# Kernel tuning notes

Hardware: AMD Instinct MI355X
Metric: run time of the kernel (lower is better)

Reference implementation:

```python
import jax, jax.numpy as jnp
import numpy as np

WD, WH, WW = 1, 8, 8           # window size
NH = 2                          # num heads
EPS = 1e-5                      # torch LayerNorm default


def _layernorm(x, g, b):
    mu = jnp.mean(x, axis=-1, keepdims=True)
    var = jnp.mean((x - mu) ** 2, axis=-1, keepdims=True)
    return (x - mu) * jax.lax.rsqrt(var + EPS) * g + b


def setup_inputs() -> dict:
    key = jax.random.key(0)
    ks = jax.random.split(key, 12)
    C, H = 192, 768  # dim, mlp hidden
    w = lambda k, shape: (jax.random.normal(k, shape, jnp.float32) * 0.02)
    return {
        "x": jax.random.normal(ks[0], (2, 8, 96, 96, C), jnp.float32),
        "norm3_g": jnp.ones((C,), jnp.float32),
        "norm3_b": jnp.zeros((C,), jnp.float32),
        "in_proj_w": w(ks[1], (3 * C, C)),
        "in_proj_b": jnp.zeros((3 * C,), jnp.float32),
        "out_proj_w": w(ks[2], (C, C)),
        "out_proj_b": jnp.zeros((C,), jnp.float32),
        "norm4_g": jnp.ones((C,), jnp.float32),
        "norm4_b": jnp.zeros((C,), jnp.float32),
        "fc1_w": w(ks[3], (H, C)),
        "fc1_b": jnp.zeros((H,), jnp.float32),
        "fc2_w": w(ks[4], (C, H)),
        "fc2_b": jnp.zeros((C,), jnp.float32),
    }


def _part3(x, norm3_g, norm3_b, in_proj_w, in_proj_b, out_proj_w, out_proj_b):
    B, D, H, W, C = x.shape
    Dn, Hn, Wn = D // WD, H // WH, W // WW
    P = Hn * Wn          # spatial windows
    Wt = WD * WH * WW    # tokens per window (64)
    L = Dn * Wt          # attention sequence length

    xn = _layernorm(x, norm3_g, norm3_b)
    # window partition: (B, Dn, Hn, Wn, wd, wh, ww, C)
    xw = xn.reshape(B, Dn, WD, Hn, WH, Wn, WW, C).transpose(0, 1, 3, 5, 2, 4, 6, 7)
    # tgt: (B, Dn, P, Wt, C) -> h: (B*P, Dn*Wt, C)
    tgt = xw.reshape(B, Dn, P, Wt, C)
    h = tgt.transpose(0, 2, 1, 3, 4).reshape(B * P, L, C)

    # qkv projection (torch Linear convention: x @ W.T + b)
    qkv = h @ in_proj_w.T + in_proj_b          # (Bp, L, 3C)
    q, k, v = jnp.split(qkv, 3, axis=-1)
    hd = C // NH
    q = q.reshape(B * P, L, NH, hd)
    k = k.reshape(B * P, L, NH, hd)
    v = v.reshape(B * P, L, NH, hd)

    # block-causal mask over temporal index (each block is Wt x Wt)
    neg_inf = jnp.finfo(jnp.float32).min
    tmask = jnp.triu(jnp.full((Dn, Dn), neg_inf, jnp.float32), k=1)
    mask = jnp.repeat(jnp.repeat(tmask, Wt, axis=0), Wt, axis=1)  # (L, L)

    scale = 1.0 / np.sqrt(hd)
    scores = jnp.einsum("blhd,bmhd->bhlm", q * scale, k) + mask
    attn = jax.nn.softmax(scores, axis=-1)
    out = jnp.einsum("bhlm,bmhd->blhd", attn, v).reshape(B * P, L, C)
    out = out @ out_proj_w.T + out_proj_b

    # reverse: (B, P, Dn, Wt, C) -> windows -> (B, D, H, W, C)
    out = out.reshape(B, P, Dn, Wt, C).transpose(0, 2, 1, 3, 4)
    out = out.reshape(B, Dn, Hn, Wn, WD, WH, WW, C)
    out = out.transpose(0, 1, 4, 2, 5, 3, 6, 7).reshape(B, D, H, W, C)
    return out


def reference(x, norm3_g, norm3_b, in_proj_w, in_proj_b, out_proj_w, out_proj_b,
              norm4_g, norm4_b, fc1_w, fc1_b, fc2_w, fc2_b):
    x = x + _part3(x, norm3_g, norm3_b, in_proj_w, in_proj_b, out_proj_w, out_proj_b)
    xn = _layernorm(x, norm4_g, norm4_b)
    mlp = jax.nn.gelu(xn @ fc1_w.T + fc1_b, approximate=False) @ fc2_w.T + fc2_b
    return x + mlp
```

## Files before the change

kernel.cpp:

```cpp
#include <hip/hip_runtime.h>
#include <cstdint>
#include <cstddef>


typedef float   f32x4  __attribute__((ext_vector_type(4)));
typedef __bf16  bf16x8 __attribute__((ext_vector_type(8)));
typedef unsigned int   u32x4  __attribute__((ext_vector_type(4)));
typedef unsigned short u16x4  __attribute__((ext_vector_type(4)));

#define DEVI __device__ __forceinline__

DEVI float bf2f(unsigned short u) {
    union { unsigned int i; float f; } v; v.i = ((unsigned int)u) << 16; return v.f;
}
DEVI unsigned short f2bf(float f) {
    unsigned int u = __builtin_bit_cast(unsigned int, f);
    unsigned int r = u + 0x7fffu + ((u >> 16) & 1u);
    return (unsigned short)(r >> 16);
}
DEVI float gelu_sig(float v) {
    float e = __expf(-1.702f * v);
    return v * __builtin_amdgcn_rcpf(1.f + e);
}
DEVI unsigned int pk_fp8x4(float a, float b, float c, float d) {
    int v = __builtin_amdgcn_cvt_pk_fp8_f32(a, b, 0, false);
    v = __builtin_amdgcn_cvt_pk_fp8_f32(c, d, v, true);
    return (unsigned int)v;
}
DEVI f32x4 mfma_fp8(unsigned long long a, unsigned long long b, f32x4 c) {
    return __builtin_amdgcn_mfma_f32_16x16x32_fp8_fp8((long)a, (long)b, c, 0, 0, 0);
}

typedef __attribute__((address_space(3))) unsigned char       lds_u8;
typedef __attribute__((address_space(1))) const unsigned char g_u8;
DEVI void gl_lds16(const void* g, void* l) {
    __builtin_amdgcn_global_load_lds((g_u8*)g, (lds_u8*)l, 16, 0, 0);
}

__global__ __launch_bounds__(256) void k_wconv(const float* __restrict__ wqkv,
                                               const float* __restrict__ wout,
                                               const float* __restrict__ wfc1,
                                               const float* __restrict__ wfc2,
                                               const float* __restrict__ n3g,
                                               const float* __restrict__ n4g,
                                               unsigned short* __restrict__ oq,
                                               unsigned short* __restrict__ oo,
                                               unsigned short* __restrict__ o1,
                                               unsigned short* __restrict__ o2f8) {
    int i = blockIdx.x * 256 + threadIdx.x;
    if (i < 122880) {
        int r = i / 192, c = i - r * 192;
        oq[i] = (r < 576) ? f2bf(wqkv[i] * n3g[c]) : (unsigned short)0;
    } else if (i < 172032) {
        int j = i - 122880; int r = j / 192;
        oo[j] = (r < 192) ? f2bf(wout[j]) : (unsigned short)0;
    } else if (i < 319488) {
        int j = i - 172032; int c = j % 192;
        o1[j] = f2bf(wfc1[j] * n4g[c]);
    } else if (i < 417792) {
        int j = i - 319488;
        int r = j / 384;
        float a = 0.f, b = 0.f;
        if (r < 192) { a = wfc2[2 * j]; b = wfc2[2 * j + 1]; }
        int pk = __builtin_amdgcn_cvt_pk_fp8_f32(a, b, 0, false);
        o2f8[j] = (unsigned short)pk;
    }
}

__global__ __launch_bounds__(256) void k_bias(const float* __restrict__ wqkv,
                                              const float* __restrict__ bqkv,
                                              const float* __restrict__ n3b,
                                              const float* __restrict__ wfc1,
                                              const float* __restrict__ bfc1,
                                              const float* __restrict__ n4b,
                                              float* __restrict__ beffq,
                                              float* __restrict__ beff1) {
    int wid = blockIdx.x * 4 + (threadIdx.x >> 6);
    int lane = threadIdx.x & 63;
    const float* wrow; const float* bb; float base; float* dst;
    if (wid < 576) { wrow = wqkv + (size_t)wid * 192; bb = n3b; base = bqkv[wid]; dst = beffq + wid; }
    else { int h = wid - 576; wrow = wfc1 + (size_t)h * 192; bb = n4b; base = bfc1[h]; dst = beff1 + h; }
    float s = wrow[lane] * bb[lane] + wrow[lane + 64] * bb[lane + 64]
            + wrow[lane + 128] * bb[lane + 128];
#pragma unroll
    for (int off = 32; off; off >>= 1) s += __shfl_xor(s, off);
    if (lane == 0) *dst = base + s;
}

__global__ __launch_bounds__(256) void k_ln3(const float* __restrict__ x,
                                             unsigned short* __restrict__ h) {
    int w = threadIdx.x >> 6, lane = threadIdx.x & 63;
    int token = blockIdx.x * 4 + w;
    const float* xp = x + (size_t)token * 192;
    float v0 = xp[lane], v1 = xp[lane + 64], v2 = xp[lane + 128];
    float s = v0 + v1 + v2;
#pragma unroll
    for (int off = 32; off; off >>= 1) s += __shfl_xor(s, off);
    float mean = s * (1.f / 192.f);
    float d0 = v0 - mean, d1 = v1 - mean, d2 = v2 - mean;
    float q = d0 * d0 + d1 * d1 + d2 * d2;
#pragma unroll
    for (int off = 32; off; off >>= 1) q += __shfl_xor(q, off);
    float rs = rsqrtf(q * (1.f / 192.f) + 1e-5f);
    int b  = token / (8 * 96 * 96);
    int r0 = token - b * (8 * 96 * 96);
    int d  = r0 / (96 * 96);
    int r1 = r0 - d * (96 * 96);
    int hh = r1 / 96;
    int ww = r1 - hh * 96;
    int bp = b * 144 + (hh >> 3) * 12 + (ww >> 3);
    int l  = d * 64 + (hh & 7) * 8 + (ww & 7);
    unsigned short* hp = h + ((size_t)bp * 512 + l) * 192;
    hp[lane]       = f2bf(d0 * rs);
    hp[lane + 64]  = f2bf(d1 * rs);
    hp[lane + 128] = f2bf(d2 * rs);
}

__global__ __launch_bounds__(256) void k_ln4b(const unsigned short* __restrict__ yb,
                                              unsigned short* __restrict__ xn) {
    int sub = threadIdx.x >> 5, tl = threadIdx.x & 31;
    size_t row = (size_t)blockIdx.x * 8 + sub;
    const unsigned int* rp = reinterpret_cast<const unsigned int*>(yb + row * 192);
    float v[6];
#pragma unroll
    for (int j = 0; j < 3; j++) {
        unsigned int w = rp[tl + 32 * j];
        v[2 * j]     = bf2f((unsigned short)(w & 0xffffu));
        v[2 * j + 1] = bf2f((unsigned short)(w >> 16));
    }
    float s = v[0] + v[1] + v[2] + v[3] + v[4] + v[5];
#pragma unroll
    for (int off = 1; off < 32; off <<= 1) s += __shfl_xor(s, off);
    float mean = s * (1.f / 192.f);
    float q = 0.f;
#pragma unroll
    for (int j = 0; j < 6; j++) { v[j] -= mean; q += v[j] * v[j]; }
#pragma unroll
    for (int off = 1; off < 32; off <<= 1) q += __shfl_xor(q, off);
    float rs = rsqrtf(q * (1.f / 192.f) + 1e-5f);
    unsigned int* op = reinterpret_cast<unsigned int*>(xn + row * 192);
#pragma unroll
    for (int j = 0; j < 3; j++) {
        unsigned short lo = f2bf(v[2 * j]     * rs);
        unsigned short hi = f2bf(v[2 * j + 1] * rs);
        op[tl + 32 * j] = ((unsigned int)hi << 16) | lo;
    }
}

template <int EPI, int K, int NF>
__global__ __launch_bounds__(256) void k_gemm128(const unsigned short* __restrict__ A,
                                                 const unsigned short* __restrict__ Bw,
                                                 const float* __restrict__ bias,
                                                 unsigned short* __restrict__ outb,
                                                 unsigned short* __restrict__ vt,
                                                 const float* __restrict__ res,
                                                 unsigned char* __restrict__ outf8) {
    __shared__ unsigned short As[2][128 * 64];
    __shared__ unsigned short Bs[2][NF * 32 * 64];
    const int tid = threadIdx.x;
    const int nwg = gridDim.x * gridDim.y;
    const int flat = blockIdx.y * gridDim.x + blockIdx.x;
    const int swz = (flat & 7) * (nwg >> 3) + (flat >> 3);
    const int bx = swz % gridDim.x, by = swz / gridDim.x;
    const int row0 = by * 128, col0 = bx * (NF * 32);
    const int wv = tid >> 6, lane = tid & 63, lr = lane & 15, lg = lane >> 4;
    const int wr = wv >> 1, wc = wv & 1;
    const int sr = lane >> 3, sc = lane & 7;
    f32x4 acc[4][NF] = {};

    auto stage = [&](int t, int buf) {
        int k0 = t * 64;
#pragma unroll
        for (int i = 0; i < 4; i++) {
            int gq = wv * 4 + i;
            int r = gq * 8 + sr;
            int j = sc ^ (r & 7);
            gl_lds16(A + (size_t)(row0 + r) * K + k0 + j * 8, &As[buf][gq * 512]);
        }
#pragma unroll
        for (int i = 0; i < NF; i++) {
            int gq = wv * NF + i;
            int r = gq * 8 + sr;
            int j = sc ^ (r & 7);
            gl_lds16(Bw + (size_t)(col0 + r) * K + k0 + j * 8, &Bs[buf][gq * 512]);
        }
    };

    const int NT = K / 64;
    stage(0, 0);
    for (int t = 0; t < NT; ++t) {
        int cur = t & 1;
        if (t + 1 < NT) {
            stage(t + 1, cur ^ 1);
            if constexpr (NF == 4) asm volatile("s_waitcnt vmcnt(8)" ::: "memory");
            else                   asm volatile("s_waitcnt vmcnt(7)" ::: "memory");
        } else {
            asm volatile("s_waitcnt vmcnt(0)" ::: "memory");
        }
        __builtin_amdgcn_sched_barrier(0);
        __builtin_amdgcn_s_barrier();
        __builtin_amdgcn_sched_barrier(0);
#pragma unroll
        for (int kk = 0; kk < 64; kk += 32) {
            bf16x8 af[4], bf[NF];
#pragma unroll
            for (int m = 0; m < 4; m++) {
                int r = wr * 64 + m * 16 + lr;
                int j = ((kk >> 3) + lg) ^ (r & 7);
                af[m] = __builtin_bit_cast(bf16x8,
                    *reinterpret_cast<const u32x4*>(&As[cur][r * 64 + j * 8]));
            }
#pragma unroll
            for (int n = 0; n < NF; n++) {
                int r = wc * (NF * 16) + n * 16 + lr;
                int j = ((kk >> 3) + lg) ^ (r & 7);
                bf[n] = __builtin_bit_cast(bf16x8,
                    *reinterpret_cast<const u32x4*>(&Bs[cur][r * 64 + j * 8]));
            }
#pragma unroll
            for (int m = 0; m < 4; m++)
#pragma unroll
                for (int n = 0; n < NF; n++)
                    acc[m][n] = __builtin_amdgcn_mfma_f32_16x16x32_bf16(bf[n], af[m], acc[m][n], 0, 0, 0);
        }
        __builtin_amdgcn_sched_barrier(0);
        __builtin_amdgcn_s_barrier();
        __builtin_amdgcn_sched_barrier(0);
    }

#pragma unroll
    for (int m = 0; m < 4; m++) {
        const int arow = row0 + wr * 64 + m * 16 + lr;
        if constexpr (EPI == 0) {
#pragma unroll
            for (int n = 0; n < NF; n++) {
                const int colb = col0 + wc * (NF * 16) + n * 16 + lg * 4;
                if (colb < 384) {
                    f32x4 b4 = *reinterpret_cast<const f32x4*>(bias + colb);
                    float sc2 = (colb < 192) ? 0.1020620726159658f : 1.f;
                    u16x4 pk;
#pragma unroll
                    for (int rr = 0; rr < 4; rr++) pk[rr] = f2bf((acc[m][n][rr] + b4[rr]) * sc2);
                    *reinterpret_cast<u16x4*>(outb + (size_t)arow * 384 + colb) = pk;
                } else if (colb < 576) {
                    int head = (colb >= 480) ? 1 : 0;
                    int bp = arow >> 9, tok = arow & 511;
                    size_t vb = ((size_t)(bp * 2 + head) * 96 + (colb - 384 - head * 96)) * 512 + tok;
#pragma unroll
                    for (int rr = 0; rr < 4; rr++)
                        vt[vb + (size_t)rr * 512] = f2bf(acc[m][n][rr] + bias[colb + rr]);
                }
            }
        } else if constexpr (EPI == 1) {
            int bp = arow >> 9, l = arow & 511;
            int bb = bp / 144, p = bp - bb * 144;
            int hn = p / 12, wn = p - hn * 12;
            int dn = l >> 6, t_ = l & 63;
            size_t tok = ((size_t)((bb * 8 + dn) * 96 + hn * 8 + (t_ >> 3)) * 96 + wn * 8 + (t_ & 7));
#pragma unroll
            for (int n = 0; n < NF; n++) {
                const int colb = col0 + wc * (NF * 16) + n * 16 + lg * 4;
                size_t idx = tok * 192 + colb;
                f32x4 r4 = *reinterpret_cast<const f32x4*>(res + idx);
                f32x4 b4 = *reinterpret_cast<const f32x4*>(bias + colb);
                u16x4 pk;
#pragma unroll
                for (int rr = 0; rr < 4; rr++) pk[rr] = f2bf(r4[rr] + acc[m][n][rr] + b4[rr]);
                *reinterpret_cast<u16x4*>(outb + idx) = pk;
            }
        } else {
#pragma unroll
            for (int n = 0; n < NF; n++) {
                const int colb = col0 + wc * (NF * 16) + n * 16 + lg * 4;
                f32x4 b4 = *reinterpret_cast<const f32x4*>(bias + colb);
                float g0 = gelu_sig(acc[m][n][0] + b4[0]);
                float g1 = gelu_sig(acc[m][n][1] + b4[1]);
                float g2 = gelu_sig(acc[m][n][2] + b4[2]);
                float g3 = gelu_sig(acc[m][n][3] + b4[3]);
                *reinterpret_cast<unsigned int*>(outf8 + (size_t)arow * 768 + colb) =
                    pk_fp8x4(g0, g1, g2, g3);
            }
        }
    }
}

__global__ __launch_bounds__(512) void k_attn(const unsigned short* __restrict__ qk,
                                              const unsigned short* __restrict__ vt,
                                              unsigned short* __restrict__ aout) {
    __shared__ unsigned short Ks[64][104];
    __shared__ unsigned short Vs[96][72];
    __shared__ unsigned short Ps[8][16][72];

    int bid = (blockIdx.x & 7) * 288 + (blockIdx.x >> 3);
    int bp = bid >> 3, rest = bid & 7, head = rest >> 2, pr = rest & 3;
    int tid = threadIdx.x, wv = tid >> 6, lane = tid & 63;
    int lr = lane & 15, lg = lane >> 4;
    int wq = wv & 3, wt = wv >> 2;
    int nk = 2 * pr + 2;

    size_t qrow0 = (size_t)bp * 512 + (size_t)(2 * pr + wt) * 64;
    const unsigned short* vbase = vt + (size_t)(bp * 2 + head) * 96 * 512;
    size_t krowb = (size_t)bp * 512;

    bf16x8 qf[3];
    {
        const unsigned short* qp = qk + (qrow0 + wq * 16 + lr) * 384 + head * 96 + lg * 8;
#pragma unroll
        for (int ks = 0; ks < 3; ks++)
            qf[ks] = __builtin_bit_cast(bf16x8, *reinterpret_cast<const u32x4*>(qp + ks * 32));
    }

    f32x4 o[6] = {};
    float m_ = -1e30f, lsum = 0.f;

    u32x4 sreg[3];
    auto issue = [&](int dnk) {
#pragma unroll
        for (int i = 0; i < 3; i++) {
            int c = tid + i * 512;
            if (c < 768) {
                int r = c / 12, cc = c - r * 12;
                sreg[i] = *reinterpret_cast<const u32x4*>(
                    qk + (krowb + dnk * 64 + r) * 384 + 192 + head * 96 + cc * 8);
            } else {
                int c2 = c - 768; int d = c2 >> 3, tb = c2 & 7;
                sreg[i] = *reinterpret_cast<const u32x4*>(
                    vbase + (size_t)d * 512 + dnk * 64 + tb * 8);
            }
        }
    };
    auto commit = [&]() {
#pragma unroll
        for (int i = 0; i < 3; i++) {
            int c = tid + i * 512;
            if (c < 768) {
                int r = c / 12, cc = c - r * 12;
                *reinterpret_cast<u32x4*>(&Ks[r][cc * 8]) = sreg[i];
            } else {
                int c2 = c - 768; int d = c2 >> 3, tb = c2 & 7;
                *reinterpret_cast<u32x4*>(&Vs[d][tb * 8]) = sreg[i];
            }
        }
    };

    issue(0);
    for (int dnk = 0; dnk < nk; ++dnk) {
        commit();
        __syncthreads();
        if (dnk + 1 < nk) issue(dnk + 1);
        if (wt == 1 || dnk < nk - 1) {
            f32x4 st[4] = {};
#pragma unroll
            for (int ks = 0; ks < 3; ks++) {
#pragma unroll
                for (int ct = 0; ct < 4; ct++) {
                    bf16x8 kf = __builtin_bit_cast(bf16x8,
                        *reinterpret_cast<const u32x4*>(&Ks[ct * 16 + lr][ks * 32 + lg * 8]));
                    st[ct] = __builtin_amdgcn_mfma_f32_16x16x32_bf16(kf, qf[ks], st[ct], 0, 0, 0);
                }
            }
            float mx = st[0][0];
#pragma unroll
            for (int ct = 0; ct < 4; ct++)
#pragma unroll
                for (int rr = 0; rr < 4; rr++) mx = fmaxf(mx, st[ct][rr]);
            mx = fmaxf(mx, __shfl_xor(mx, 16));
            mx = fmaxf(mx, __shfl_xor(mx, 32));
            float mnew = fmaxf(m_, mx);
            float corr = __expf(m_ - mnew);
            m_ = mnew;
            float ps = 0.f;
#pragma unroll
            for (int ct = 0; ct < 4; ct++) {
                u16x4 pk;
#pragma unroll
                for (int rr = 0; rr < 4; rr++) {
                    float pv = __expf(st[ct][rr] - mnew);
                    ps += pv;
                    pk[rr] = f2bf(pv);
                }
                *reinterpret_cast<u16x4*>(&Ps[wv][lr][ct * 16 + lg * 4]) = pk;
            }
            ps += __shfl_xor(ps, 16);
            ps += __shfl_xor(ps, 32);
            lsum = lsum * corr + ps;
#pragma unroll
            for (int rr = 0; rr < 4; rr++) {
                float cr = __shfl(corr, (lane & 48) | (lg * 4 + rr));
#pragma unroll
                for (int nf = 0; nf < 6; nf++) o[nf][rr] *= cr;
            }
#pragma unroll
            for (int kk = 0; kk < 2; kk++) {
                bf16x8 pf = __builtin_bit_cast(bf16x8,
                    *reinterpret_cast<const u32x4*>(&Ps[wv][lr][kk * 32 + lg * 8]));
#pragma unroll
                for (int nf = 0; nf < 6; nf++) {
                    bf16x8 vf = __builtin_bit_cast(bf16x8,
                        *reinterpret_cast<const u32x4*>(&Vs[nf * 16 + lr][kk * 32 + lg * 8]));
                    o[nf] = __builtin_amdgcn_mfma_f32_16x16x32_bf16(pf, vf, o[nf], 0, 0, 0);
                }
            }
        }
        __syncthreads();
    }

#pragma unroll
    for (int rr = 0; rr < 4; rr++) {
        float li = __shfl(lsum, (lane & 48) | (lg * 4 + rr));
        float inv = 1.f / li;
        size_t row = qrow0 + wq * 16 + lg * 4 + rr;
#pragma unroll
        for (int nf = 0; nf < 6; nf++)
            aout[row * 192 + head * 96 + nf * 16 + lr] = f2bf(o[nf][rr] * inv);
    }
}

__global__ __launch_bounds__(256) void k_fc2(const unsigned char* __restrict__ hid,
                                             const unsigned char* __restrict__ w2,
                                             const float* __restrict__ b2,
                                             const unsigned short* __restrict__ ybf,
                                             float* __restrict__ out) {
    __shared__ unsigned char As[2][128 * 64];
    __shared__ unsigned char Bs[2][128 * 64];
    const int tid = threadIdx.x;
    const int nwg = gridDim.x * gridDim.y;
    const int flat = blockIdx.y * gridDim.x + blockIdx.x;
    const int swz = (flat & 7) * (nwg >> 3) + (flat >> 3);
    const int bx = swz % gridDim.x, by = swz / gridDim.x;
    const int row0 = by * 128, col0 = bx * 96;
    const int wv = tid >> 6, lane = tid & 63, lr = lane & 15, lg = lane >> 4;
    const int wr = wv >> 1, wc = wv & 1;
    const int sr4 = lane >> 2, sc4 = lane & 3;
    f32x4 acc[4][3] = {};

    auto stage = [&](int t, int buf) {
        int k0 = t * 64;
#pragma unroll
        for (int i = 0; i < 2; i++) {
            int g = wv * 2 + i;
            int r = g * 16 + sr4;
            int j = sc4 ^ (r & 3);
            gl_lds16(hid + (size_t)(row0 + r) * 768 + k0 + j * 16, &As[buf][g * 1024]);
        }
#pragma unroll
        for (int i = 0; i < 2; i++) {
            int g = wv * 2 + i;
            int r = g * 16 + sr4;
            int j = sc4 ^ (r & 3);
            gl_lds16(w2 + (size_t)(col0 + r) * 768 + k0 + j * 16, &Bs[buf][g * 1024]);
        }
    };

    stage(0, 0);
    for (int t = 0; t < 12; ++t) {
        int cur = t & 1;
        if (t + 1 < 12) {
            stage(t + 1, cur ^ 1);
            asm volatile("s_waitcnt vmcnt(4)" ::: "memory");
        } else {
            asm volatile("s_waitcnt vmcnt(0)" ::: "memory");
        }
        __builtin_amdgcn_sched_barrier(0);
        __builtin_amdgcn_s_barrier();
        __builtin_amdgcn_sched_barrier(0);
#pragma unroll
        for (int kk = 0; kk < 2; kk++) {
            const int cc = kk * 2 + (lg >> 1);
            const int off = (lg & 1) * 8;
            unsigned long long af[4], bfr[3];
#pragma unroll
            for (int m = 0; m < 4; m++) {
                int r = wr * 64 + m * 16 + lr;
                int j = cc ^ (r & 3);
                af[m] = *reinterpret_cast<const unsigned long long*>(
                    &As[cur][r * 64 + j * 16 + off]);
            }
#pragma unroll
            for (int n = 0; n < 3; n++) {
                int r = wc * 48 + n * 16 + lr;
                int j = cc ^ (r & 3);
                bfr[n] = *reinterpret_cast<const unsigned long long*>(
                    &Bs[cur][r * 64 + j * 16 + off]);
            }
#pragma unroll
            for (int m = 0; m < 4; m++)
#pragma unroll
                for (int n = 0; n < 3; n++)
                    acc[m][n] = mfma_fp8(bfr[n], af[m], acc[m][n]);
        }
        __builtin_amdgcn_sched_barrier(0);
        __builtin_amdgcn_s_barrier();
        __builtin_amdgcn_sched_barrier(0);
    }

#pragma unroll
    for (int m = 0; m < 4; m++) {
        const int arow = row0 + wr * 64 + m * 16 + lr;
#pragma unroll
        for (int n = 0; n < 3; n++) {
            const int colb = col0 + wc * 48 + n * 16 + lg * 4;
            size_t idx = (size_t)arow * 192 + colb;
            f32x4 b4 = *reinterpret_cast<const f32x4*>(b2 + colb);
            u16x4 rb = *reinterpret_cast<const u16x4*>(ybf + idx);
            f32x4 o4;
#pragma unroll
            for (int rr = 0; rr < 4; rr++) o4[rr] = bf2f(rb[rr]) + acc[m][n][rr] + b4[rr];
            *reinterpret_cast<f32x4*>(out + idx) = o4;
        }
    }
}

extern "C" void kernel_launch(void* const* d_in, const int* in_sizes, int n_in,
                              void* d_out, int out_size, void* d_ws, size_t ws_size,
                              hipStream_t stream) {
    const float* x    = (const float*)d_in[0];
    const float* n3g  = (const float*)d_in[1];
    const float* n3b  = (const float*)d_in[2];
    const float* wqkv = (const float*)d_in[3];
    const float* bqkv = (const float*)d_in[4];
    const float* wout = (const float*)d_in[5];
    const float* bout = (const float*)d_in[6];
    const float* n4g  = (const float*)d_in[7];
    const float* n4b  = (const float*)d_in[8];
    const float* wfc1 = (const float*)d_in[9];
    const float* bfc1 = (const float*)d_in[10];
    const float* wfc2 = (const float*)d_in[11];
    const float* bfc2 = (const float*)d_in[12];
    float* out = (float*)d_out;

    char* ws = (char*)d_ws;
    unsigned short* qk     = (unsigned short*)(ws + 0);
    unsigned char*  hidden = (unsigned char*)(ws + 0);
    unsigned short* vt     = (unsigned short*)(ws + 113246208);
    unsigned short* attn   = (unsigned short*)(ws + 169869312);
    unsigned short* ybf    = (unsigned short*)(ws + 226492416);
    unsigned short* h      = (unsigned short*)(ws + 283115520);
    unsigned short* xn4    = (unsigned short*)(ws + 283115520);
    unsigned short* wq_bf  = (unsigned short*)(ws + 339738624);
    unsigned short* wo_bf  = (unsigned short*)(ws + 339984384);
    unsigned short* w1_bf  = (unsigned short*)(ws + 340082688);
    unsigned short* w2_f8p = (unsigned short*)(ws + 340377600);
    unsigned char*  w2_f8  = (unsigned char*)(ws + 340377600);
    float*          beffq  = (float*)(ws + 340574208);
    float*          beff1  = (float*)(ws + 340576512);

    k_wconv<<<1632, 256, 0, stream>>>(wqkv, wout, wfc1, wfc2, n3g, n4g, wq_bf, wo_bf, w1_bf, w2_f8p);
    k_bias<<<336, 256, 0, stream>>>(wqkv, bqkv, n3b, wfc1, bfc1, n4b, beffq, beff1);
    k_ln3<<<36864, 256, 0, stream>>>(x, h);
    k_gemm128<0, 192, 4><<<dim3(5, 1152), 256, 0, stream>>>(h, wq_bf, beffq, qk, vt, nullptr, nullptr);
    k_attn<<<2304, 512, 0, stream>>>(qk, vt, attn);
    k_gemm128<1, 192, 3><<<dim3(2, 1152), 256, 0, stream>>>(attn, wo_bf, bout, ybf, nullptr, x, nullptr);
    k_ln4b<<<18432, 256, 0, stream>>>(ybf, xn4);
    k_gemm128<2, 192, 4><<<dim3(6, 1152), 256, 0, stream>>>(xn4, w1_bf, beff1, nullptr, nullptr, nullptr, hidden);
    k_fc2<<<dim3(2, 1152), 256, 0, stream>>>(hidden, w2_f8, bfc2, ybf, out);
}
```

Baseline: 513.6 us.

## Fold LayerNorm4 into fc1 epilogue via row stats and triple-buffer fc2 loads

Instead of writing a normalized bf16 copy of the residual before fc1, a small kernel now computes only each row's mean and rstd. fc1 reads the raw bf16 residual and corrects the result algebraically in its epilogue using (acc - mean*sum(W*g))*rstd + bias. This removes one full activation write and re-read, at the cost of GEMM precision on non-centered inputs and a few extra epilogue loads. Separately, the fc2 kernel moves from double to triple buffering in shared memory to prefetch two k-tiles ahead.

Measured after the change: 516.1 us. No clear change (+0.5%).

```diff
diff --git a/kernel.cpp b/kernel.cpp
--- a/kernel.cpp
+++ b/kernel.cpp
@@ -4,6 +4,7 @@
 
 
 typedef float   f32x4  __attribute__((ext_vector_type(4)));
+typedef float   f32x2  __attribute__((ext_vector_type(2)));
 typedef __bf16  bf16x8 __attribute__((ext_vector_type(8)));
 typedef unsigned int   u32x4  __attribute__((ext_vector_type(4)));
 typedef unsigned short u16x4  __attribute__((ext_vector_type(4)));
@@ -73,18 +74,30 @@
                                               const float* __restrict__ wfc1,
                                               const float* __restrict__ bfc1,
                                               const float* __restrict__ n4b,
+                                              const float* __restrict__ n4g,
                                               float* __restrict__ beffq,
-                                              float* __restrict__ beff1) {
+                                              float* __restrict__ beff1,
+                                              float* __restrict__ w1sum) {
     int wid = blockIdx.x * 4 + (threadIdx.x >> 6);
     int lane = threadIdx.x & 63;
-    const float* wrow; const float* bb; float base; float* dst;
-    if (wid < 576) { wrow = wqkv + (size_t)wid * 192; bb = n3b; base = bqkv[wid]; dst = beffq + wid; }
-    else { int h = wid - 576; wrow = wfc1 + (size_t)h * 192; bb = n4b; base = bfc1[h]; dst = beff1 + h; }
-    float s = wrow[lane] * bb[lane] + wrow[lane + 64] * bb[lane + 64]
-            + wrow[lane + 128] * bb[lane + 128];
-#pragma unroll
-    for (int off = 32; off; off >>= 1) s += __shfl_xor(s, off);
-    if (lane == 0) *dst = base + s;
+    if (wid < 576) {
+        const float* wrow = wqkv + (size_t)wid * 192;
+        float s = wrow[lane] * n3b[lane] + wrow[lane + 64] * n3b[lane + 64]
+                + wrow[lane + 128] * n3b[lane + 128];
+#pragma unroll
+        for (int off = 32; off; off >>= 1) s += __shfl_xor(s, off);
+        if (lane == 0) beffq[wid] = bqkv[wid] + s;
+    } else {
+        int h = wid - 576;
+        const float* wrow = wfc1 + (size_t)h * 192;
+        float s = wrow[lane] * n4b[lane] + wrow[lane + 64] * n4b[lane + 64]
+                + wrow[lane + 128] * n4b[lane + 128];
+        float s2 = wrow[lane] * n4g[lane] + wrow[lane + 64] * n4g[lane + 64]
+                 + wrow[lane + 128] * n4g[lane + 128];
+#pragma unroll
+        for (int off = 32; off; off >>= 1) { s += __shfl_xor(s, off); s2 += __shfl_xor(s2, off); }
+        if (lane == 0) { beff1[h] = bfc1[h] + s; w1sum[h] = s2; }
+    }
 }
 
 __global__ __launch_bounds__(256) void k_ln3(const float* __restrict__ x,
@@ -116,8 +129,8 @@
     hp[lane + 128] = f2bf(d2 * rs);
 }
 
-__global__ __launch_bounds__(256) void k_ln4b(const unsigned short* __restrict__ yb,
-                                              unsigned short* __restrict__ xn) {
+__global__ __launch_bounds__(256) void k_stats(const unsigned short* __restrict__ yb,
+                                               float* __restrict__ st) {
     int sub = threadIdx.x >> 5, tl = threadIdx.x & 31;
     size_t row = (size_t)blockIdx.x * 8 + sub;
     const unsigned int* rp = reinterpret_cast<const unsigned int*>(yb + row * 192);
@@ -134,17 +147,11 @@
     float mean = s * (1.f / 192.f);
     float q = 0.f;
 #pragma unroll
-    for (int j = 0; j < 6; j++) { v[j] -= mean; q += v[j] * v[j]; }
+    for (int j = 0; j < 6; j++) { float d = v[j] - mean; q += d * d; }
 #pragma unroll
     for (int off = 1; off < 32; off <<= 1) q += __shfl_xor(q, off);
     float rs = rsqrtf(q * (1.f / 192.f) + 1e-5f);
-    unsigned int* op = reinterpret_cast<unsigned int*>(xn + row * 192);
-#pragma unroll
-    for (int j = 0; j < 3; j++) {
-        unsigned short lo = f2bf(v[2 * j]     * rs);
-        unsigned short hi = f2bf(v[2 * j + 1] * rs);
-        op[tl + 32 * j] = ((unsigned int)hi << 16) | lo;
-    }
+    if (tl == 0) { st[row * 2] = mean; st[row * 2 + 1] = rs; }
 }
 
 template <int EPI, int K, int NF>
@@ -154,7 +161,9 @@
                                                  unsigned short* __restrict__ outb,
                                                  unsigned short* __restrict__ vt,
                                                  const float* __restrict__ res,
-                                                 unsigned char* __restrict__ outf8) {
+                                                 unsigned char* __restrict__ outf8,
+                                                 const float* __restrict__ stats,
+                                                 const float* __restrict__ wsum) {
     __shared__ unsigned short As[2][128 * 64];
     __shared__ unsigned short Bs[2][NF * 32 * 64];
     const int tid = threadIdx.x;
@@ -269,14 +278,16 @@
                 *reinterpret_cast<u16x4*>(outb + idx) = pk;
             }
         } else {
+            f32x2 st = *reinterpret_cast<const f32x2*>(stats + 2 * arow);
 #pragma unroll
             for (int n = 0; n < NF; n++) {
                 const int colb = col0 + wc * (NF * 16) + n * 16 + lg * 4;
                 f32x4 b4 = *reinterpret_cast<const f32x4*>(bias + colb);
-                float g0 = gelu_sig(acc[m][n][0] + b4[0]);
-                float g1 = gelu_sig(acc[m][n][1] + b4[1]);
-                float g2 = gelu_sig(acc[m][n][2] + b4[2]);
-                float g3 = gelu_sig(acc[m][n][3] + b4[3]);
+                f32x4 S4 = *reinterpret_cast<const f32x4*>(wsum + colb);
+                float g0 = gelu_sig((acc[m][n][0] - st[0] * S4[0]) * st[1] + b4[0]);
+                float g1 = gelu_sig((acc[m][n][1] - st[0] * S4[1]) * st[1] + b4[1]);
+                float g2 = gelu_sig((acc[m][n][2] - st[0] * S4[2]) * st[1] + b4[2]);
+                float g3 = gelu_sig((acc[m][n][3] - st[0] * S4[3]) * st[1] + b4[3]);
                 *reinterpret_cast<unsigned int*>(outf8 + (size_t)arow * 768 + colb) =
                     pk_fp8x4(g0, g1, g2, g3);
             }
@@ -421,8 +432,8 @@
                                              const float* __restrict__ b2,
                                              const unsigned short* __restrict__ ybf,
                                              float* __restrict__ out) {
-    __shared__ unsigned char As[2][128 * 64];
-    __shared__ unsigned char Bs[2][128 * 64];
+    __shared__ unsigned char As[3][128 * 64];
+    __shared__ unsigned char Bs[3][128 * 64];
     const int tid = threadIdx.x;
     const int nwg = gridDim.x * gridDim.y;
     const int flat = blockIdx.y * gridDim.x + blockIdx.x;
@@ -453,10 +464,13 @@
     };
 
     stage(0, 0);
+    stage(1, 1);
+    int cur = 0;
     for (int t = 0; t < 12; ++t) {
-        int cur = t & 1;
-        if (t + 1 < 12) {
-            stage(t + 1, cur ^ 1);
+        if (t + 2 < 12) {
+            stage(t + 2, (t + 2) % 3);
+            asm volatile("s_waitcnt vmcnt(8)" ::: "memory");
+        } else if (t + 1 < 12) {
             asm volatile("s_waitcnt vmcnt(4)" ::: "memory");
         } else {
             asm volatile("s_waitcnt vmcnt(0)" ::: "memory");
@@ -492,6 +506,7 @@
         __builtin_amdgcn_sched_barrier(0);
         __builtin_amdgcn_s_barrier();
         __builtin_amdgcn_sched_barrier(0);
+        cur = (cur + 1) % 3;
     }
 
 #pragma unroll
@@ -536,7 +551,6 @@
     unsigned short* attn   = (unsigned short*)(ws + 169869312);
     unsigned short* ybf    = (unsigned short*)(ws + 226492416);
     unsigned short* h      = (unsigned short*)(ws + 283115520);
-    unsigned short* xn4    = (unsigned short*)(ws + 283115520);
     unsigned short* wq_bf  = (unsigned short*)(ws + 339738624);
     unsigned short* wo_bf  = (unsigned short*)(ws + 339984384);
     unsigned short* w1_bf  = (unsigned short*)(ws + 340082688);
@@ -544,14 +558,16 @@
     unsigned char*  w2_f8  = (unsigned char*)(ws + 340377600);
     float*          beffq  = (float*)(ws + 340574208);
     float*          beff1  = (float*)(ws + 340576512);
+    float*          w1sum  = (float*)(ws + 340579584);
+    float*          stats  = (float*)(ws + 340582656);
 
     k_wconv<<<1632, 256, 0, stream>>>(wqkv, wout, wfc1, wfc2, n3g, n4g, wq_bf, wo_bf, w1_bf, w2_f8p);
-    k_bias<<<336, 256, 0, stream>>>(wqkv, bqkv, n3b, wfc1, bfc1, n4b, beffq, beff1);
+    k_bias<<<336, 256, 0, stream>>>(wqkv, bqkv, n3b, wfc1, bfc1, n4b, n4g, beffq, beff1, w1sum);
     k_ln3<<<36864, 256, 0, stream>>>(x, h);
-    k_gemm128<0, 192, 4><<<dim3(5, 1152), 256, 0, stream>>>(h, wq_bf, beffq, qk, vt, nullptr, nullptr);
+    k_gemm128<0, 192, 4><<<dim3(5, 1152), 256, 0, stream>>>(h, wq_bf, beffq, qk, vt, nullptr, nullptr, nullptr, nullptr);
     k_attn<<<2304, 512, 0, stream>>>(qk, vt, attn);
-    k_gemm128<1, 192, 3><<<dim3(2, 1152), 256, 0, stream>>>(attn, wo_bf, bout, ybf, nullptr, x, nullptr);
-    k_ln4b<<<18432, 256, 0, stream>>>(ybf, xn4);
-    k_gemm128<2, 192, 4><<<dim3(6, 1152), 256, 0, stream>>>(xn4, w1_bf, beff1, nullptr, nullptr, nullptr, hidden);
+    k_gemm128<1, 192, 3><<<dim3(2, 1152), 256, 0, stream>>>(attn, wo_bf, bout, ybf, nullptr, x, nullptr, nullptr, nullptr);
+    k_stats<<<18432, 256, 0, stream>>>(ybf, stats);
+    k_gemm128<2, 192, 4><<<dim3(6, 1152), 256, 0, stream>>>(ybf, w1_bf, beff1, nullptr, nullptr, nullptr, hidden, stats, w1sum);
     k_fc2<<<dim3(2, 1152), 256, 0, stream>>>(hidden, w2_f8, bfc2, ybf, out);
 }
```
